# Kernel tuning notes

Hardware: AMD Instinct MI355X
Metric: run time of the kernel (lower is better)

The kernel has to match this reference:

```python
import jax, jax.numpy as jnp
import numpy as np

# Model hyperparameters (match init_kwargs)
K = 4          # number of experts (branches)
STEPS = 3
TOP_N = 2
HEADS = 2
DIM_HEAD = 64
ROUTE_TEMP = 1.5
C = 256        # channels


def conv3x3(x, w, b):
    # x: [B,H,W,Cin], w: [3,3,Cin,Cout], b: [Cout]
    y = jax.lax.conv_general_dilated(
        x, w, window_strides=(1, 1), padding='SAME',
        dimension_numbers=('NHWC', 'HWIO', 'NHWC'))
    return y + b


def setup_inputs() -> dict:
    key = jax.random.key(0)
    ks = jax.random.split(key, 8)
    B, H, W = 32, 32, 32
    D = HEADS * DIM_HEAD  # 128
    glorot = jax.nn.initializers.glorot_uniform()
    x = jax.random.normal(ks[0], (B, H, W, C), dtype=jnp.float32)
    q = glorot(ks[1], (HEADS, DIM_HEAD), jnp.float32)          # router queries
    Wk = glorot(ks[2], (C, D), jnp.float32)                    # 1x1 conv key proj
    Wv = glorot(ks[3], (C, D), jnp.float32)                    # 1x1 conv val proj
    Wmlp = glorot(ks[4], (D, K), jnp.float32)                  # head_mlp (mlp_hidden=0)
    alpha = jnp.zeros((), jnp.float32)                         # attn_log_alpha
    We = glorot(ks[5], (K * 3, 3, C, C), jnp.float32).reshape(K, 3, 3, C, C)
    be = jnp.zeros((K, C), jnp.float32)
    return {"x": x, "q": q, "Wk": Wk, "Wv": Wv, "Wmlp": Wmlp,
            "alpha": alpha, "We": We, "be": be}


def reference(x, q, Wk, Wv, Wmlp, alpha, We, be):
    B, H, W, Cc = x.shape
    S = H * W
    allowed = jnp.ones((B, K), x.dtype)
    last_oh = jax.nn.one_hot(jnp.full((B,), K - 1), K, dtype=x.dtype)
    scale = jnp.asarray(S, x.dtype)
    a = jax.nn.softplus(alpha)

    for t in range(STEPS):
        # ---- AttnPoolRouter ----
        k = jnp.einsum('bhwc,cd->bhwd', x, Wk).reshape(B, S, HEADS, DIM_HEAD)
        v = jnp.einsum('bhwc,cd->bhwd', x, Wv).reshape(B, S, HEADS, DIM_HEAD)
        # attention logits: [B, heads, S]
        attn = jax.nn.softmax(
            jnp.einsum('nd,bsnd->bns', q, k) / jnp.sqrt(jnp.asarray(DIM_HEAD, x.dtype)),
            axis=-1)
        pooled = jnp.einsum('bns,bsnd->bnd', attn, v).reshape(B, HEADS * DIM_HEAD)
        logits = pooled @ Wmlp                                   # [B, K]
        attn_map = attn.mean(axis=1).reshape(B, H, W, 1)

        # ---- routing with exclusion mask ----
        masked_logits = jnp.where(allowed > 0.5, logits, jnp.asarray(-1e9, x.dtype))
        weights = jax.nn.softmax(masked_logits / ROUTE_TEMP, axis=-1)
        top_vals, top_idx = jax.lax.top_k(weights, TOP_N)        # [B, n]
        mask_oh = jax.nn.one_hot(top_idx, K, dtype=x.dtype).sum(axis=1)  # [B, K]
        wm = weights * mask_oh
        wsel = wm / (wm.sum(axis=-1, keepdims=True) + 1e-9)      # == straight-through fwd value

        # ---- modulate input and run selected experts (dense-equivalent) ----
        x_mod = x * (1.0 + attn_map * scale * a)
        y = jnp.zeros_like(x)
        for e in range(K):
            ye = conv3x3(x_mod, We[e], be[e])
            y = y + wsel[:, e][:, None, None, None] * ye

        # ---- update allowed: disallow step top-1 unless it's the last expert ----
        top1 = top_idx[:, 0]
        not_last = (top1 != K - 1).astype(x.dtype)
        delta = jax.nn.one_hot(top1, K, dtype=x.dtype) * not_last[:, None]
        allowed = jnp.clip(allowed - delta, 0.0, 1.0)
        allowed = jnp.maximum(allowed, last_oh)
        x = y
    return x
```

## Files before the change

### kernel.cpp

```cpp
#include <hip/hip_runtime.h>

typedef _Float16 f16x8 __attribute__((ext_vector_type(8)));
typedef __fp16 fp16x2 __attribute__((ext_vector_type(2)));
typedef __attribute__((ext_vector_type(4))) float f32x4;

#define CC 256
#define SS 1024
#define KK 4
#define XR 6
#define XC 34
#define NCELL (XR * XC)

__device__ __forceinline__ unsigned int pk2h(float a, float b) {
  fp16x2 h = __builtin_amdgcn_cvt_pkrtz(a, b);
  return __builtin_bit_cast(unsigned int, h);
}

__device__ __forceinline__ void gll16(const void* g, void* l) {
  __builtin_amdgcn_global_load_lds((const __attribute__((address_space(1))) void*)g,
                                   (__attribute__((address_space(3))) void*)l, 16, 0, 0);
}

#define S_VMCNT0 asm volatile("s_waitcnt vmcnt(0)" ::: "memory")
#define S_LGKM0 asm volatile("s_waitcnt lgkmcnt(0)" ::: "memory")
#define SCHED0 __builtin_amdgcn_sched_barrier(0)

__global__ void qk_kernel(const float* __restrict__ Wk, const float* __restrict__ q,
                          float* __restrict__ qk) {
  int t = blockIdx.x * blockDim.x + threadIdx.x;
  if (t >= CC * 2) return;
  int c = t >> 1, n = t & 1;
  float s = 0.f;
  for (int d = 0; d < 64; ++d) s += Wk[c * 128 + n * 64 + d] * q[n * 64 + d];
  qk[c * 2 + n] = s;
}

__global__ void poolpart_kernel(const float* __restrict__ x, const float* __restrict__ qk,
                                float* __restrict__ scores, float* __restrict__ part) {
  __shared__ float xs[64][260];
  __shared__ float ds[2][64];
  int ch = blockIdx.x, b = blockIdx.y, tid = threadIdx.x;
  int s0 = ch * 64;
  const float* xb = x + ((size_t)b * 1024 + s0) * 256;
  for (int i = tid; i < 4096; i += 256) {
    int r = i >> 6, c4 = (i & 63) << 2;
    *(float4*)(&xs[r][c4]) = *(const float4*)(xb + (size_t)r * 256 + c4);
  }
  __syncthreads();
  int lane = tid & 63, wv = tid >> 6;
  float q0[4], q1[4];
#pragma unroll
  for (int j = 0; j < 4; ++j) {
    q0[j] = qk[(lane + j * 64) * 2 + 0];
    q1[j] = qk[(lane + j * 64) * 2 + 1];
  }
  for (int p = 0; p < 16; ++p) {
    int s = wv * 16 + p;
    float d0 = 0.f, d1 = 0.f;
#pragma unroll
    for (int j = 0; j < 4; ++j) {
      float xv = xs[s][lane + j * 64];
      d0 += xv * q0[j];
      d1 += xv * q1[j];
    }
#pragma unroll
    for (int sh = 32; sh >= 1; sh >>= 1) {
      d0 += __shfl_xor(d0, sh, 64);
      d1 += __shfl_xor(d1, sh, 64);
    }
    if (lane == 0) {
      ds[0][s] = d0 * 0.125f;
      ds[1][s] = d1 * 0.125f;
      scores[((size_t)b * 2 + 0) * 1024 + s0 + s] = d0 * 0.125f;
      scores[((size_t)b * 2 + 1) * 1024 + s0 + s] = d1 * 0.125f;
    }
  }
  __syncthreads();
  if (wv < 2) {
    float v = ds[wv][lane];
    float m = v;
#pragma unroll
    for (int sh = 32; sh >= 1; sh >>= 1) m = fmaxf(m, __shfl_xor(m, sh, 64));
    float e = expf(v - m);
    float Z = e;
#pragma unroll
    for (int sh = 32; sh >= 1; sh >>= 1) Z += __shfl_xor(Z, sh, 64);
    ds[wv][lane] = e;
    if (lane == 0) {
      float* o = part + ((size_t)(b * 16 + ch)) * 520;
      o[wv] = m;
      o[2 + wv] = Z;
    }
  }
  __syncthreads();
  float a0 = 0.f, a1 = 0.f;
  for (int s = 0; s < 64; ++s) {
    float xv = xs[s][tid];
    a0 += ds[0][s] * xv;
    a1 += ds[1][s] * xv;
  }
  float* o = part + ((size_t)(b * 16 + ch)) * 520;
  o[4 + tid] = a0;
  o[4 + 256 + tid] = a1;
}

__global__ void route_kernel(const float* __restrict__ part, const float* __restrict__ scores,
                             const float* __restrict__ Wv, const float* __restrict__ Wmlp,
                             const float* __restrict__ alpha, float* __restrict__ allowed,
                             float* __restrict__ rowscale,
                             int* __restrict__ selE, float* __restrict__ selW, int step) {
  __shared__ float xs[512];
  __shared__ float pooled[128];
  __shared__ float lg[4];
  __shared__ float Msh[2], iZsh[2];
  int b = blockIdx.x, tid = threadIdx.x;
  if (tid < 2) {
    float m = -1e30f;
    for (int ch = 0; ch < 16; ++ch)
      m = fmaxf(m, part[((size_t)(b * 16 + ch)) * 520 + tid]);
    float z = 0.f;
    for (int ch = 0; ch < 16; ++ch) {
      const float* p = part + ((size_t)(b * 16 + ch)) * 520;
      z += expf(p[tid] - m) * p[2 + tid];
    }
    Msh[tid] = m;
    iZsh[tid] = 1.f / z;
  }
  __syncthreads();
  float M0 = Msh[0], M1 = Msh[1], iZ0 = iZsh[0], iZ1 = iZsh[1];
  {
    float al = alpha[0];
    float a = (al > 20.f) ? al : log1pf(expf(al));
    float k = 0.5f * 1024.f * a;
    for (int i = tid; i < 1024; i += 256) {
      float d0 = scores[((size_t)b * 2 + 0) * 1024 + i];
      float d1 = scores[((size_t)b * 2 + 1) * 1024 + i];
      rowscale[(size_t)b * 1024 + i] = 1.f + k * (expf(d0 - M0) * iZ0 + expf(d1 - M1) * iZ1);
    }
  }
#pragma unroll
  for (int i = 0; i < 2; ++i) {
    int id = tid + i * 256;
    int n = id >> 8, c = id & 255;
    float s = 0.f;
    for (int ch = 0; ch < 16; ++ch) {
      const float* p = part + ((size_t)(b * 16 + ch)) * 520;
      s += expf(p[n] - Msh[n]) * p[4 + n * 256 + c];
    }
    xs[id] = s * iZsh[n];
  }
  __syncthreads();
  if (tid < 128) {
    int n = tid >> 6;
    float s = 0.f;
    const float* xr = xs + n * 256;
    for (int c = 0; c < 256; ++c) s += xr[c] * Wv[(size_t)c * 128 + tid];
    pooled[tid] = s;
  }
  __syncthreads();
  if (tid < 4) {
    float s = 0.f;
    for (int d = 0; d < 128; ++d) s += pooled[d] * Wmlp[d * 4 + tid];
    lg[tid] = s;
  }
  __syncthreads();
  if (tid == 0) {
    float al[KK];
    if (step == 0) { for (int k = 0; k < KK; ++k) al[k] = 1.f; }
    else           { for (int k = 0; k < KK; ++k) al[k] = allowed[b * KK + k]; }
    float ml[KK];
    for (int k = 0; k < KK; ++k)
      ml[k] = (al[k] > 0.5f) ? lg[k] * (1.f / 1.5f) : (-1e9f) * (1.f / 1.5f);
    float m = ml[0];
    for (int k = 1; k < KK; ++k) m = fmaxf(m, ml[k]);
    float e[KK], ssum = 0.f;
    for (int k = 0; k < KK; ++k) { e[k] = expf(ml[k] - m); ssum += e[k]; }
    float w[KK];
    for (int k = 0; k < KK; ++k) w[k] = e[k] / ssum;
    int i0 = 0;
    for (int k = 1; k < KK; ++k) if (w[k] > w[i0]) i0 = k;
    int i1 = -1;
    for (int k = 0; k < KK; ++k) {
      if (k == i0) continue;
      if (i1 < 0 || w[k] > w[i1]) i1 = k;
    }
    float denom = w[i0] + w[i1] + 1e-9f;
    selE[b * 2 + 0] = i0;
    selE[b * 2 + 1] = i1;
    selW[b * 2 + 0] = w[i0] / denom;
    selW[b * 2 + 1] = w[i1] / denom;
    if (i0 != KK - 1) al[i0] = fminf(fmaxf(al[i0] - 1.f, 0.f), 1.f);
    al[KK - 1] = fmaxf(al[KK - 1], 1.f);
    for (int k = 0; k < KK; ++k) allowed[b * KK + k] = al[k];
  }
}

__global__ void combine_w_kernel(const float* __restrict__ We,
                                 const int* __restrict__ selE, const float* __restrict__ selW,
                                 unsigned short* __restrict__ Wc_h) {
  int tile = blockIdx.x;
  int b = blockIdx.y;
  int tap = tile >> 3, kc = tile & 7;
  int co = threadIdx.x;
  int e0 = selE[b * 2], e1 = selE[b * 2 + 1];
  float w0 = selW[b * 2], w1 = selW[b * 2 + 1];
  __shared__ float ts[32][257];
  const float* s0 = We + (size_t)(e0 * 9 + tap) * 65536 + (size_t)(kc * 32) * 256 + co;
  const float* s1 = We + (size_t)(e1 * 9 + tap) * 65536 + (size_t)(kc * 32) * 256 + co;
  for (int ci = 0; ci < 32; ++ci)
    ts[ci][co] = w0 * s0[(size_t)ci * 256] + w1 * s1[(size_t)ci * 256];
  __syncthreads();
  unsigned int hw[16];
#pragma unroll
  for (int k2 = 0; k2 < 16; ++k2) hw[k2] = pk2h(ts[k2 * 2][co], ts[k2 * 2 + 1][co]);
  size_t base = ((size_t)b * 72 + tile) * 8192 + (size_t)co * 32;
#pragma unroll
  for (int j = 0; j < 4; ++j)
    *(uint4*)(Wc_h + base + j * 8) = make_uint4(hw[j * 4], hw[j * 4 + 1], hw[j * 4 + 2], hw[j * 4 + 3]);
}

__global__ __launch_bounds__(256, 2) void conv_kernel(
    const float* __restrict__ xin, const float* __restrict__ rowscale,
    const unsigned short* __restrict__ Wc_h,
    const float* __restrict__ be,
    const int* __restrict__ selE, const float* __restrict__ selW,
    float* __restrict__ out) {
  __shared__ __align__(16) unsigned char xsB[2][NCELL * 64];
  __shared__ __align__(16) unsigned char BsB[2][3 * 8192];
  __shared__ float rs_lds[NCELL];

  int bid = blockIdx.x;
  int xcd = bid & 7, t2b = bid >> 3;
  int mt = t2b & 7, gs = t2b >> 3;
  int g = gs * 8 + xcd;
  int b = g >> 1, nt = g & 1;
  int h0 = mt * 4;
  int tid = threadIdx.x;
  int lane = tid & 63, wid = tid >> 6;
  int wm = wid >> 1, wn = wid & 1;
  int l15 = lane & 15, kl = lane >> 4;

  int e0 = selE[b * 2], e1 = selE[b * 2 + 1];
  float w0 = selW[b * 2], w1 = selW[b * 2 + 1];

  int cellb[4];
#pragma unroll
  for (int mf = 0; mf < 4; ++mf) {
    int p0 = wm * 64 + mf * 16;
    cellb[mf] = (p0 >> 5) * XC + (p0 & 31) + l15;
  }
  int bbyte[4];
#pragma unroll
  for (int nf = 0; nf < 4; ++nf) {
    int co = wn * 64 + nf * 16 + l15;
    bbyte[nf] = (co * 64 + kl * 16) ^ ((co & 7) << 4);
  }
  int elemoff[2];
#pragma unroll
  for (int j = 0; j < 2; ++j) {
    int oh = wid * 2048 + j * 1024 + lane * 16;
    int co = ((oh >> 7) << 1) | (((oh >> 6) ^ (oh >> 8)) & 1);
    int s = ((oh >> 4) & 3) ^ (co & 3);
    elemoff[j] = (nt * 128 + co) * 32 + s * 8;
  }
  const unsigned short* WH = Wc_h + (size_t)b * 72 * 8192;

  float bias[4];
#pragma unroll
  for (int nf = 0; nf < 4; ++nf) {
    int con = nt * 128 + wn * 64 + nf * 16 + l15;
    bias[nf] = w0 * be[e0 * 256 + con] + w1 * be[e1 * 256 + con];
  }

  f32x4 acc[4][4];
#pragma unroll
  for (int mf = 0; mf < 4; ++mf)
#pragma unroll
    for (int nf = 0; nf < 4; ++nf) acc[mf][nf] = (f32x4){0.f, 0.f, 0.f, 0.f};

  for (int i = tid; i < NCELL; i += 256) {
    int r = i / XC, c = i - r * XC;
    int gr = h0 - 1 + r, gc = c - 1;
    float v = 0.f;
    if (gr >= 0 && gr < 32 && gc >= 0 && gc < 32)
      v = rowscale[(size_t)b * 1024 + gr * 32 + gc];
    rs_lds[i] = v;
  }

  auto stage_x = [&](int kcc) {
    unsigned char* xd = xsB[kcc & 1];
    for (int idx = tid; idx < NCELL * 2; idx += 256) {
      int hk = (idx >= NCELL) ? 1 : 0;
      int cell = idx - hk * NCELL;
      int r = cell / XC, c = cell - r * XC;
      int gr = h0 - 1 + r, gc = c - 1;
      uint4 pk = make_uint4(0, 0, 0, 0), pk2 = make_uint4(0, 0, 0, 0);
      if (gr >= 0 && gr < 32 && gc >= 0 && gc < 32) {
        const float* src = xin + (((size_t)b * 32 + gr) * 32 + gc) * 256 + kcc * 32 + hk * 16;
        float sc = rs_lds[cell];
        float xv[16];
        *(float4*)(xv + 0) = *(const float4*)(src + 0);
        *(float4*)(xv + 4) = *(const float4*)(src + 4);
        *(float4*)(xv + 8) = *(const float4*)(src + 8);
        *(float4*)(xv + 12) = *(const float4*)(src + 12);
        unsigned int u[8];
#pragma unroll
        for (int e2 = 0; e2 < 8; ++e2)
          u[e2] = pk2h(xv[e2 * 2] * sc, xv[e2 * 2 + 1] * sc);
        pk = make_uint4(u[0], u[1], u[2], u[3]);
        pk2 = make_uint4(u[4], u[5], u[6], u[7]);
      }
      int sx = (cell & 7) << 4;
      int b0 = (cell * 64 + hk * 32) ^ sx;
      int b1 = (cell * 64 + hk * 32 + 16) ^ sx;
      *(uint4*)(xd + b0) = pk;
      *(uint4*)(xd + b1) = pk2;
    }
  };

  auto issue_group = [&](int kcA, int subBase, int buf) {
#pragma unroll
    for (int t = 0; t < 3; ++t) {
      const unsigned short* sp = WH + (size_t)((subBase + t) * 8 + kcA) * 8192;
      char* lb = (char*)&BsB[buf][t * 8192] + wid * 2048;
      gll16(sp + elemoff[0], lb);
      gll16(sp + elemoff[1], lb + 1024);
    }
    SCHED0;
  };

  auto do_tap = [&](int tap, int tIdx, const unsigned char* xsCur, int buf) {
    const int dy = (tap >= 6) ? 2 : ((tap >= 3) ? 1 : 0);
    const int dx = tap - dy * 3;
    const int dcell = dy * XC + dx;
    const unsigned char* bp = &BsB[buf][tIdx * 8192];
    f16x8 af[4], bf[4];
#pragma unroll
    for (int mf = 0; mf < 4; ++mf) {
      int cell = cellb[mf] + dcell;
      int abyte = (cell * 64 + kl * 16) ^ ((cell & 7) << 4);
      af[mf] = *(const f16x8*)(xsCur + abyte);
    }
#pragma unroll
    for (int nf = 0; nf < 4; ++nf) bf[nf] = *(const f16x8*)(bp + bbyte[nf]);
    __builtin_amdgcn_s_setprio(1);
#pragma unroll
    for (int mf = 0; mf < 4; ++mf)
#pragma unroll
      for (int nf = 0; nf < 4; ++nf)
        acc[mf][nf] = __builtin_amdgcn_mfma_f32_16x16x32_f16(af[mf], bf[nf], acc[mf][nf], 0, 0, 0);
    __builtin_amdgcn_s_setprio(0);
  };

  issue_group(0, 0, 0);
  __syncthreads();
  stage_x(0);
  S_VMCNT0;
  S_LGKM0;
  SCHED0;
  __builtin_amdgcn_s_barrier();

#pragma unroll 1
  for (int kc = 0; kc < 8; ++kc) {
    const unsigned char* xsCur = xsB[kc & 1];
    const int bX = kc & 1;
    if (kc < 7) stage_x(kc + 1);
    issue_group(kc, 3, bX ^ 1);
    do_tap(0, 0, xsCur, bX);
    do_tap(1, 1, xsCur, bX);
    do_tap(2, 2, xsCur, bX);
    S_VMCNT0;
    SCHED0;
    __builtin_amdgcn_s_barrier();
    issue_group(kc, 6, bX);
    do_tap(3, 0, xsCur, bX ^ 1);
    do_tap(4, 1, xsCur, bX ^ 1);
    do_tap(5, 2, xsCur, bX ^ 1);
    S_VMCNT0;
    SCHED0;
    __builtin_amdgcn_s_barrier();
    if (kc < 7) issue_group(kc + 1, 0, bX ^ 1);
    do_tap(6, 0, xsCur, bX);
    do_tap(7, 1, xsCur, bX);
    do_tap(8, 2, xsCur, bX);
    if (kc < 7) { S_LGKM0; }
    S_VMCNT0;
    SCHED0;
    __builtin_amdgcn_s_barrier();
  }

#pragma unroll
  for (int mf = 0; mf < 4; ++mf) {
    int p0 = wm * 64 + mf * 16;
    int pr = p0 >> 5, pc = p0 & 31;
    size_t rowbase = ((size_t)b * 32 + h0 + pr) * 32;
#pragma unroll
    for (int nf = 0; nf < 4; ++nf) {
      int co = nt * 128 + wn * 64 + nf * 16 + l15;
#pragma unroll
      for (int rr = 0; rr < 4; ++rr) {
        int col = pc + kl * 4 + rr;
        out[(rowbase + col) * 256 + co] = acc[mf][nf][rr] + bias[nf];
      }
    }
  }
}

extern "C" void kernel_launch(void* const* d_in, const int* in_sizes, int n_in,
                              void* d_out, int out_size, void* d_ws, size_t ws_size,
                              hipStream_t stream) {
  const float* x_in  = (const float*)d_in[0];
  const float* q     = (const float*)d_in[1];
  const float* Wk    = (const float*)d_in[2];
  const float* Wv    = (const float*)d_in[3];
  const float* Wmlp  = (const float*)d_in[4];
  const float* alpha = (const float*)d_in[5];
  const float* We    = (const float*)d_in[6];
  const float* be    = (const float*)d_in[7];
  float* out = (float*)d_out;
  float* ws = (float*)d_ws;

  float* qk       = ws;
  float* scores   = qk + 512;
  float* rowscale = scores + 65536;
  float* part     = rowscale + 32768;
  float* allowed  = part + 266240;
  float* selW     = allowed + 128;
  int*   selE     = (int*)(selW + 64);
  float* xbuf     = selW + 128;
  unsigned short* Wc_h = (unsigned short*)(xbuf + 8388608);

  qk_kernel<<<2, 256, 0, stream>>>(Wk, q, qk);

  const float* step_in[3] = {x_in, out, xbuf};
  float* step_out[3] = {out, xbuf, out};

  for (int t = 0; t < 3; ++t) {
    const float* xc = step_in[t];
    poolpart_kernel<<<dim3(16, 32), 256, 0, stream>>>(xc, qk, scores, part);
    route_kernel<<<32, 256, 0, stream>>>(part, scores, Wv, Wmlp, alpha, allowed, rowscale, selE, selW, t);
    combine_w_kernel<<<dim3(72, 32), 256, 0, stream>>>(We, selE, selW, Wc_h);
    conv_kernel<<<512, 256, 0, stream>>>(xc, rowscale, Wc_h, be, selE, selW, step_out[t]);
  }
}
```

Measured before the change: 304.0 us.

## Fuse routing into weight-combine kernel by recomputing route per tile block

Merges route_kernel and combine_w_kernel into one launch: each of the 72 tile blocks per batch recomputes the routing decision (pooling, Wv projection, MLP, top-2) redundantly, then combines expert weights. Rowscale computation is split across the first 8 tiles and the allowed mask is double-buffered to avoid read/write races between blocks. This removes one kernel launch and its serialization per step, at the cost of 72x redundant router work (including a 256x128 Wv matvec per block).

```diff
diff --git a/kernel.cpp b/kernel.cpp
--- a/kernel.cpp
+++ b/kernel.cpp
@@ -104,16 +104,25 @@
   o[4 + 256 + tid] = a1;
 }
 
-__global__ void route_kernel(const float* __restrict__ part, const float* __restrict__ scores,
-                             const float* __restrict__ Wv, const float* __restrict__ Wmlp,
-                             const float* __restrict__ alpha, float* __restrict__ allowed,
-                             float* __restrict__ rowscale,
-                             int* __restrict__ selE, float* __restrict__ selW, int step) {
+__global__ void routecombine_kernel(
+    const float* __restrict__ part, const float* __restrict__ scores,
+    const float* __restrict__ Wv, const float* __restrict__ Wmlp,
+    const float* __restrict__ alpha, const float* __restrict__ We,
+    const float* __restrict__ allowed_in, float* __restrict__ allowed_out,
+    float* __restrict__ rowscale, int* __restrict__ selE, float* __restrict__ selW,
+    unsigned short* __restrict__ Wc_h, int step) {
+  __shared__ float ts[32][257];
   __shared__ float xs[512];
   __shared__ float pooled[128];
   __shared__ float lg[4];
   __shared__ float Msh[2], iZsh[2];
-  int b = blockIdx.x, tid = threadIdx.x;
+  __shared__ float cs[2][16];
+  __shared__ int sel_sh[2];
+  __shared__ float sw_sh[2];
+  int tile = blockIdx.x;
+  int b = blockIdx.y;
+  int tid = threadIdx.x;
+
   if (tid < 2) {
     float m = -1e30f;
     for (int ch = 0; ch < 16; ++ch)
@@ -127,26 +136,18 @@
     iZsh[tid] = 1.f / z;
   }
   __syncthreads();
-  float M0 = Msh[0], M1 = Msh[1], iZ0 = iZsh[0], iZ1 = iZsh[1];
-  {
-    float al = alpha[0];
-    float a = (al > 20.f) ? al : log1pf(expf(al));
-    float k = 0.5f * 1024.f * a;
-    for (int i = tid; i < 1024; i += 256) {
-      float d0 = scores[((size_t)b * 2 + 0) * 1024 + i];
-      float d1 = scores[((size_t)b * 2 + 1) * 1024 + i];
-      rowscale[(size_t)b * 1024 + i] = 1.f + k * (expf(d0 - M0) * iZ0 + expf(d1 - M1) * iZ1);
-    }
-  }
+  if (tid < 32) {
+    int n = tid >> 4, ch = tid & 15;
+    cs[n][ch] = expf(part[((size_t)(b * 16 + ch)) * 520 + n] - Msh[n]);
+  }
+  __syncthreads();
 #pragma unroll
   for (int i = 0; i < 2; ++i) {
     int id = tid + i * 256;
     int n = id >> 8, c = id & 255;
     float s = 0.f;
-    for (int ch = 0; ch < 16; ++ch) {
-      const float* p = part + ((size_t)(b * 16 + ch)) * 520;
-      s += expf(p[n] - Msh[n]) * p[4 + n * 256 + c];
-    }
+    for (int ch = 0; ch < 16; ++ch)
+      s += cs[n][ch] * part[((size_t)(b * 16 + ch)) * 520 + 4 + n * 256 + c];
     xs[id] = s * iZsh[n];
   }
   __syncthreads();
@@ -167,7 +168,7 @@
   if (tid == 0) {
     float al[KK];
     if (step == 0) { for (int k = 0; k < KK; ++k) al[k] = 1.f; }
-    else           { for (int k = 0; k < KK; ++k) al[k] = allowed[b * KK + k]; }
+    else           { for (int k = 0; k < KK; ++k) al[k] = allowed_in[b * KK + k]; }
     float ml[KK];
     for (int k = 0; k < KK; ++k)
       ml[k] = (al[k] > 0.5f) ? lg[k] * (1.f / 1.5f) : (-1e9f) * (1.f / 1.5f);
@@ -185,26 +186,36 @@
       if (i1 < 0 || w[k] > w[i1]) i1 = k;
     }
     float denom = w[i0] + w[i1] + 1e-9f;
-    selE[b * 2 + 0] = i0;
-    selE[b * 2 + 1] = i1;
-    selW[b * 2 + 0] = w[i0] / denom;
-    selW[b * 2 + 1] = w[i1] / denom;
-    if (i0 != KK - 1) al[i0] = fminf(fmaxf(al[i0] - 1.f, 0.f), 1.f);
-    al[KK - 1] = fmaxf(al[KK - 1], 1.f);
-    for (int k = 0; k < KK; ++k) allowed[b * KK + k] = al[k];
-  }
-}
-
-__global__ void combine_w_kernel(const float* __restrict__ We,
-                                 const int* __restrict__ selE, const float* __restrict__ selW,
-                                 unsigned short* __restrict__ Wc_h) {
-  int tile = blockIdx.x;
-  int b = blockIdx.y;
+    sel_sh[0] = i0;
+    sel_sh[1] = i1;
+    sw_sh[0] = w[i0] / denom;
+    sw_sh[1] = w[i1] / denom;
+    if (tile == 0) {
+      selE[b * 2 + 0] = i0;
+      selE[b * 2 + 1] = i1;
+      selW[b * 2 + 0] = sw_sh[0];
+      selW[b * 2 + 1] = sw_sh[1];
+      if (i0 != KK - 1) al[i0] = fminf(fmaxf(al[i0] - 1.f, 0.f), 1.f);
+      al[KK - 1] = fmaxf(al[KK - 1], 1.f);
+      for (int k = 0; k < KK; ++k) allowed_out[b * KK + k] = al[k];
+    }
+  }
+  if (tile < 8 && tid < 128) {
+    float M0 = Msh[0], M1 = Msh[1], iZ0 = iZsh[0], iZ1 = iZsh[1];
+    float alv = alpha[0];
+    float a = (alv > 20.f) ? alv : log1pf(expf(alv));
+    float k = 0.5f * 1024.f * a;
+    int i = tile * 128 + tid;
+    float d0 = scores[((size_t)b * 2 + 0) * 1024 + i];
+    float d1 = scores[((size_t)b * 2 + 1) * 1024 + i];
+    rowscale[(size_t)b * 1024 + i] = 1.f + k * (expf(d0 - M0) * iZ0 + expf(d1 - M1) * iZ1);
+  }
+  __syncthreads();
+
+  int e0 = sel_sh[0], e1 = sel_sh[1];
+  float w0 = sw_sh[0], w1 = sw_sh[1];
   int tap = tile >> 3, kc = tile & 7;
-  int co = threadIdx.x;
-  int e0 = selE[b * 2], e1 = selE[b * 2 + 1];
-  float w0 = selW[b * 2], w1 = selW[b * 2 + 1];
-  __shared__ float ts[32][257];
+  int co = tid;
   const float* s0 = We + (size_t)(e0 * 9 + tap) * 65536 + (size_t)(kc * 32) * 256 + co;
   const float* s1 = We + (size_t)(e1 * 9 + tap) * 65536 + (size_t)(kc * 32) * 256 + co;
   for (int ci = 0; ci < 32; ++ci)
@@ -424,8 +435,9 @@
   float* scores   = qk + 512;
   float* rowscale = scores + 65536;
   float* part     = rowscale + 32768;
-  float* allowed  = part + 266240;
-  float* selW     = allowed + 128;
+  float* alwA     = part + 266240;
+  float* alwB     = alwA + 128;
+  float* selW     = alwB + 128;
   int*   selE     = (int*)(selW + 64);
   float* xbuf     = selW + 128;
   unsigned short* Wc_h = (unsigned short*)(xbuf + 8388608);
@@ -434,12 +446,14 @@
 
   const float* step_in[3] = {x_in, out, xbuf};
   float* step_out[3] = {out, xbuf, out};
+  float* alw[2] = {alwA, alwB};
 
   for (int t = 0; t < 3; ++t) {
     const float* xc = step_in[t];
     poolpart_kernel<<<dim3(16, 32), 256, 0, stream>>>(xc, qk, scores, part);
-    route_kernel<<<32, 256, 0, stream>>>(part, scores, Wv, Wmlp, alpha, allowed, rowscale, selE, selW, t);
-    combine_w_kernel<<<dim3(72, 32), 256, 0, stream>>>(We, selE, selW, Wc_h);
+    routecombine_kernel<<<dim3(72, 32), 256, 0, stream>>>(
+        part, scores, Wv, Wmlp, alpha, We, alw[t & 1], alw[(t + 1) & 1],
+        rowscale, selE, selW, Wc_h, t);
     conv_kernel<<<512, 256, 0, stream>>>(xc, rowscale, Wc_h, be, selE, selW, step_out[t]);
   }
 }
```

Result: slower. 339.8 us (+11.8%).
